# Optimization experiments

Measured on AMD Instinct MI355X. Metric: run time of the kernel, lower is better.

Reference implementation:

```python
import jax, jax.numpy as jnp
import numpy as np

D_MODEL = 1024
N_HEADS = 16
D_HEAD = 64
SEQ = 2048
BATCH = 2
ATTN_SCALE = float(np.sqrt(D_HEAD))  # cfg.use_attn_scale = True
NEG_INF = -1e9


def setup_inputs() -> dict:
    key = jax.random.key(0)
    ks = jax.random.split(key, 8)
    s = 0.02
    return {
        "query_input": jax.random.normal(ks[0], (BATCH, SEQ, D_MODEL), jnp.float32),
        "key_input": jax.random.normal(ks[1], (BATCH, SEQ, D_MODEL), jnp.float32),
        "value_input": jax.random.normal(ks[2], (BATCH, SEQ, D_MODEL), jnp.float32),
        "W_Q": jax.random.normal(ks[3], (N_HEADS, D_MODEL, D_HEAD), jnp.float32) * s,
        "W_K": jax.random.normal(ks[4], (N_HEADS, D_MODEL, D_HEAD), jnp.float32) * s,
        "W_V": jax.random.normal(ks[5], (N_HEADS, D_MODEL, D_HEAD), jnp.float32) * s,
        "W_O": jax.random.normal(ks[6], (N_HEADS, D_HEAD, D_MODEL), jnp.float32) * s,
        "b_Q": jnp.zeros((N_HEADS, D_HEAD), jnp.float32),
        "b_K": jnp.zeros((N_HEADS, D_HEAD), jnp.float32),
        "b_V": jnp.zeros((N_HEADS, D_HEAD), jnp.float32),
        "b_O": jnp.zeros((D_MODEL,), jnp.float32),
    }


def reference(query_input, key_input, value_input, W_Q, W_K, W_V, W_O, b_Q, b_K, b_V, b_O):
    # QKV projections: [batch, pos, d_model] x [head, d_model, d_head] -> [batch, pos, head, d_head]
    q = jnp.einsum("bpd,hde->bphe", query_input, W_Q) + b_Q
    k = jnp.einsum("bpd,hde->bphe", key_input, W_K) + b_K
    v = jnp.einsum("bpd,hde->bphe", value_input, W_V) + b_V

    # attn scores [batch, head, query_pos, key_pos]
    scores = jnp.einsum("bqhe,bkhe->bhqk", q, k) / ATTN_SCALE

    # causal mask (attn_type == 'global'): tril over [n_ctx, n_ctx] sliced to seq
    causal = jnp.tril(jnp.ones((SEQ, SEQ), bool))
    scores = jnp.where(causal[None, None, :, :], scores, NEG_INF)

    pattern = jax.nn.softmax(scores, axis=-1)

    # z: [batch, query_pos, head, d_head]
    z = jnp.einsum("bhqk,bkhe->bqhe", pattern, v)

    # output projection: [batch, pos, d_model]
    out = jnp.einsum("bqhe,hed->bqd", z, W_O) + b_O
    return out
```

## Files before the change

kernel.cpp:

```cpp
#include <hip/hip_runtime.h>
#include <stdint.h>


typedef __attribute__((ext_vector_type(8))) short short8;
typedef __attribute__((ext_vector_type(4))) short short4v;
typedef __attribute__((ext_vector_type(4))) float floatx4;
typedef __attribute__((ext_vector_type(4))) unsigned int uintx4;
typedef __attribute__((ext_vector_type(2))) unsigned int uint2v;

#define MFMA16(a, b, c) __builtin_amdgcn_mfma_f32_16x16x32_bf16(a, b, c, 0, 0, 0)

#if __has_builtin(__builtin_amdgcn_mfma_f32_16x16x16bf16_1k)
#define HAVE_K16 1
#define MFMAK16(a, b, c) __builtin_amdgcn_mfma_f32_16x16x16bf16_1k(a, b, c, 0, 0, 0)
#else
#define HAVE_K16 0
#endif

__device__ __forceinline__ unsigned short f2b(float f) {
  unsigned int u = __builtin_bit_cast(unsigned int, f);
  u = (u + 0x7fffu + ((u >> 16) & 1u)) >> 16;
  return (unsigned short)u;
}
__device__ __forceinline__ float exp2f_fast(float x) {
#if __has_builtin(__builtin_amdgcn_exp2f)
  return __builtin_amdgcn_exp2f(x);
#else
  return exp2f(x);
#endif
}
__device__ __forceinline__ unsigned int pack2_bf16(float lo, float hi) {
#if __has_builtin(__builtin_amdgcn_perm)
  return __builtin_amdgcn_perm(__builtin_bit_cast(unsigned int, hi),
                               __builtin_bit_cast(unsigned int, lo), 0x07060302u);
#else
  return (__builtin_bit_cast(unsigned int, lo) >> 16) |
         (__builtin_bit_cast(unsigned int, hi) & 0xffff0000u);
#endif
}

__device__ __forceinline__ void async_copy16(void* lds, const void* g) {
  __builtin_amdgcn_global_load_lds(
      (const __attribute__((address_space(1))) unsigned int*)g,
      (__attribute__((address_space(3))) unsigned int*)lds, 16, 0, 0);
}

__device__ __forceinline__ void xpose4(floatx4& v, int lane) {
  {
    float s0 = __shfl_xor(v[1], 1, 64);
    float s1 = __shfl_xor(v[0], 1, 64);
    float s2 = __shfl_xor(v[3], 1, 64);
    float s3 = __shfl_xor(v[2], 1, 64);
    if (lane & 1) { v[0] = s0; v[2] = s2; } else { v[1] = s1; v[3] = s3; }
  }
  {
    float s0 = __shfl_xor(v[2], 2, 64);
    float s1 = __shfl_xor(v[3], 2, 64);
    float s2 = __shfl_xor(v[0], 2, 64);
    float s3 = __shfl_xor(v[1], 2, 64);
    if (lane & 2) { v[0] = s0; v[1] = s1; } else { v[2] = s2; v[3] = s3; }
  }
}

__global__ __launch_bounds__(256) void convall(
    const float* __restrict__ Xq, const float* __restrict__ Xk,
    const float* __restrict__ Xv, const float* __restrict__ WQ,
    const float* __restrict__ WK, const float* __restrict__ WV,
    const float* __restrict__ WO, unsigned short* __restrict__ xout,
    unsigned short* __restrict__ wout, unsigned short* __restrict__ woout) {
  __shared__ float T[64][65];
  const int bid = blockIdx.x;
  const int t = threadIdx.x;
  if (bid < 12288) {
    const int yy = bid / 4096, x = bid - yy * 4096;
    const float* in = (yy == 0) ? Xq : ((yy == 1) ? Xk : Xv);
    size_t i = (size_t)x * 256 + t;
    float4 v = ((const float4*)in)[i];
    ushort4 u;
    u.x = f2b(v.x); u.y = f2b(v.y); u.z = f2b(v.z); u.w = f2b(v.w);
    ((ushort4*)(xout + (size_t)yy * 4194304))[i] = u;
    return;
  }
  const int rr = t >> 4, cc = t & 15;
  if (bid < 13056) {
    const int sub = bid - 12288;
    const int yy = sub >> 8, x = sub & 255;
    const float* in = (yy == 0) ? WQ : ((yy == 1) ? WK : WV);
    const int h = x >> 4, d0 = (x & 15) << 6;
#pragma unroll
    for (int it = 0; it < 4; ++it) {
      int dl = it * 16 + rr;
      float4 v = *(const float4*)&in[(size_t)h * 65536 + (size_t)(d0 + dl) * 64 + cc * 4];
      T[dl][cc * 4 + 0] = v.x; T[dl][cc * 4 + 1] = v.y;
      T[dl][cc * 4 + 2] = v.z; T[dl][cc * 4 + 3] = v.w;
    }
    __syncthreads();
    unsigned short* ob = wout + (size_t)yy * 1048576;
#pragma unroll
    for (int it = 0; it < 4; ++it) {
      int e = it * 16 + rr;
      ushort4 u;
      u.x = f2b(T[cc * 4 + 0][e]); u.y = f2b(T[cc * 4 + 1][e]);
      u.z = f2b(T[cc * 4 + 2][e]); u.w = f2b(T[cc * 4 + 3][e]);
      *(ushort4*)&ob[(size_t)(h * 64 + e) * 1024 + d0 + cc * 4] = u;
    }
    return;
  }
  {
    const int x = bid - 13056;
    const int r0 = (x & 15) << 6, c0 = (x >> 4) << 6;
#pragma unroll
    for (int it = 0; it < 4; ++it) {
      int rl = it * 16 + rr;
      float4 v = *(const float4*)&WO[(size_t)(r0 + rl) * 1024 + c0 + cc * 4];
      T[rl][cc * 4 + 0] = v.x; T[rl][cc * 4 + 1] = v.y;
      T[rl][cc * 4 + 2] = v.z; T[rl][cc * 4 + 3] = v.w;
    }
    __syncthreads();
#pragma unroll
    for (int it = 0; it < 4; ++it) {
      int dl = it * 16 + rr;
      ushort4 u;
      u.x = f2b(T[cc * 4 + 0][dl]); u.y = f2b(T[cc * 4 + 1][dl]);
      u.z = f2b(T[cc * 4 + 2][dl]); u.w = f2b(T[cc * 4 + 3][dl]);
      *(ushort4*)&woout[(size_t)(c0 + dl) * 1024 + r0 + cc * 4] = u;
    }
  }
}

template <int TM, int NZ>
__global__ __launch_bounds__(512, (TM == 128) ? 6 : 4) void gemm512(
    const short* __restrict__ A0, const short* __restrict__ A1,
    const short* __restrict__ A2, const short* __restrict__ B0,
    const short* __restrict__ B1, const short* __restrict__ B2,
    const float* __restrict__ bias0, const float* __restrict__ bias1,
    const float* __restrict__ bias2, unsigned short* __restrict__ ob0,
    unsigned short* __restrict__ ob1, unsigned short* __restrict__ ob2,
    float* __restrict__ outf, float qscale) {
  constexpr int WAVES_N = (TM == 128) ? 2 : 4;
  constexpr int NJ = (TM == 128) ? 4 : 2;
  constexpr int NY = 4096 / TM;
  __shared__ short As[TM * 32];
  __shared__ short Bs[128 * 32];

  const int L = blockIdx.x;
  const int x = L / (NY * NZ);
  const int r = L - x * (NY * NZ);
  const int y = r / NZ;
  const int z = r - y * NZ;

  const short* A = (z == 0) ? A0 : (z == 1) ? A1 : A2;
  const short* Bt = (z == 0) ? B0 : (z == 1) ? B1 : B2;

  const int tid = threadIdx.x;
  const int lane = tid & 63, w = tid >> 6;
  const int quad = lane >> 4, col = lane & 15;
  const int m0 = y * TM, n0 = x * 128;
  const int wm = (w / WAVES_N) * 32, wn = (w % WAVES_N) * (NJ * 16);

  floatx4 acc[2][NJ] = {};

  const int lr = lane >> 2, gc = (lane & 3) ^ ((lane >> 3) & 3);
  const short* ga = A + (size_t)(m0 + w * 16 + lr) * 1024 + gc * 8;
  const short* gb = Bt + (size_t)(n0 + w * 16 + lr) * 1024 + gc * 8;
  const int asw = (col >> 1) & 3;
  const bool stageA = (w < TM / 16);

  for (int k0 = 0; k0 < 1024; k0 += 32) {
    if (stageA) async_copy16(&As[(w * 16) * 32], ga);
    async_copy16(&Bs[(w * 16) * 32], gb);
    ga += 32; gb += 32;
    __syncthreads();
    short8 af[2], bf[NJ];
#pragma unroll
    for (int mi = 0; mi < 2; ++mi)
      af[mi] = *(const short8*)&As[(wm + mi * 16 + col) * 32 + ((quad ^ asw) * 8)];
#pragma unroll
    for (int nj = 0; nj < NJ; ++nj)
      bf[nj] = *(const short8*)&Bs[(wn + nj * 16 + col) * 32 + ((quad ^ asw) * 8)];
#pragma unroll
    for (int mi = 0; mi < 2; ++mi)
#pragma unroll
      for (int nj = 0; nj < NJ; ++nj)
        acc[mi][nj] = MFMA16(af[mi], bf[nj], acc[mi][nj]);
    __syncthreads();
  }

  const float* bias = (z == 0) ? bias0 : (z == 1) ? bias1 : bias2;
  unsigned short* outb = (z == 0) ? ob0 : (z == 1) ? ob1 : ob2;
  const int mode = (NZ == 3) ? ((z == 2) ? 2 : 1) : 0;
  const float scale = (NZ == 3 && z == 0) ? qscale : 1.0f;

  float bv[NJ];
#pragma unroll
  for (int nj = 0; nj < NJ; ++nj) bv[nj] = bias[n0 + wn + nj * 16 + col];

  if (mode == 2) {
#pragma unroll
    for (int mi = 0; mi < 2; ++mi)
#pragma unroll
      for (int nj = 0; nj < NJ; ++nj) {
        int m = m0 + wm + mi * 16 + quad * 4;
        int n = n0 + wn + nj * 16 + col;
        int bb = m >> 11, s = m & 2047, h = n >> 6, e = n & 63;
        ushort4 u;
        u.x = f2b(acc[mi][nj][0] + bv[nj]);
        u.y = f2b(acc[mi][nj][1] + bv[nj]);
        u.z = f2b(acc[mi][nj][2] + bv[nj]);
        u.w = f2b(acc[mi][nj][3] + bv[nj]);
        *(ushort4*)&outb[(((size_t)bb * 16 + h) * 64 + e) * 2048 + s] = u;
      }
  } else {
#pragma unroll
    for (int mi = 0; mi < 2; ++mi)
#pragma unroll
      for (int nj = 0; nj < NJ; ++nj) {
        floatx4 v;
#pragma unroll
        for (int rr = 0; rr < 4; ++rr) v[rr] = (acc[mi][nj][rr] + bv[nj]) * scale;
        xpose4(v, lane);
        int m = m0 + wm + mi * 16 + quad * 4 + (col & 3);
        int nb = n0 + wn + nj * 16 + (col & ~3);
        if (mode == 0) {
          *(floatx4*)&outf[(size_t)m * 1024 + nb] = v;
        } else {
          int bb = m >> 11, s = m & 2047, h = nb >> 6, e = nb & 63;
          ushort4 u;
          u.x = f2b(v[0]); u.y = f2b(v[1]); u.z = f2b(v[2]); u.w = f2b(v[3]);
          *(ushort4*)&outb[(((size_t)bb * 16 + h) * 2048 + s) * 64 + e] = u;
        }
      }
  }
}

#if !HAVE_K16
__device__ __forceinline__ void exchange4(const unsigned int* u01,
                                          const unsigned int* u23, int srcA,
                                          int srcB, bool hiq, short8& pf0,
                                          short8& pf1) {
  unsigned int xA0 = (unsigned int)__shfl((int)u01[0], srcA, 64);
  unsigned int xA1 = (unsigned int)__shfl((int)u01[1], srcA, 64);
  unsigned int yA0 = (unsigned int)__shfl((int)u23[0], srcA, 64);
  unsigned int yA1 = (unsigned int)__shfl((int)u23[1], srcA, 64);
  unsigned int xB0 = (unsigned int)__shfl((int)u01[0], srcB, 64);
  unsigned int xB1 = (unsigned int)__shfl((int)u01[1], srcB, 64);
  unsigned int yB0 = (unsigned int)__shfl((int)u23[0], srcB, 64);
  unsigned int yB1 = (unsigned int)__shfl((int)u23[1], srcB, 64);
  uintx4 v0;
  v0.x = hiq ? xA1 : xA0; v0.y = hiq ? yA1 : yA0;
  v0.z = hiq ? xB1 : xB0; v0.w = hiq ? yB1 : yB0;
  pf0 = __builtin_bit_cast(short8, v0);
  xA0 = (unsigned int)__shfl((int)u01[2], srcA, 64);
  xA1 = (unsigned int)__shfl((int)u01[3], srcA, 64);
  yA0 = (unsigned int)__shfl((int)u23[2], srcA, 64);
  yA1 = (unsigned int)__shfl((int)u23[3], srcA, 64);
  xB0 = (unsigned int)__shfl((int)u01[2], srcB, 64);
  xB1 = (unsigned int)__shfl((int)u01[3], srcB, 64);
  yB0 = (unsigned int)__shfl((int)u23[2], srcB, 64);
  yB1 = (unsigned int)__shfl((int)u23[3], srcB, 64);
  uintx4 v1;
  v1.x = hiq ? xA1 : xA0; v1.y = hiq ? yA1 : yA0;
  v1.z = hiq ? xB1 : xB0; v1.w = hiq ? yB1 : yB0;
  pf1 = __builtin_bit_cast(short8, v1);
}
#endif

__device__ __forceinline__ void stage_kv(short* Kbuf, short* Vbuf,
                                         const short* kg, const short* vg,
                                         int kv0, int w, int slr, int sgc) {
  const short* kr = kg + (size_t)(kv0 + w * 16 + slr) * 64 + sgc * 8;
  async_copy16(&Kbuf[(w * 16) * 64], kr);
  async_copy16(&Kbuf[(w * 16 + 8) * 64], kr + 8 * 64);
  const short* vr = vg + (size_t)(w * 16 + slr) * 2048 + kv0 + sgc * 8;
  async_copy16(&Vbuf[(w * 16) * 64], vr);
  async_copy16(&Vbuf[(w * 16 + 8) * 64], vr + 8 * 2048);
}

__global__ __launch_bounds__(256) void attn(const short* __restrict__ q,
                                            const short* __restrict__ k,
                                            const short* __restrict__ vt,
                                            unsigned short* __restrict__ z) {
  __shared__ short Ks[2][64 * 64];
  __shared__ short Vs[2][64 * 64];

  const int tid = threadIdx.x;
  const int lane = tid & 63, w = tid >> 6;
  const int quad = lane >> 4, col = lane & 15;
  const int qt = 31 - (blockIdx.x >> 5), bh = blockIdx.x & 31;
  const int q0 = qt * 64, qw0 = q0 + w * 16;
  const size_t base = (size_t)bh * (2048 * 64);

  const short* qp = q + base + (size_t)(qw0 + col) * 64 + quad * 8;
  short8 bq0 = *(const short8*)qp;
  short8 bq1 = *(const short8*)(qp + 32);

  floatx4 o[4] = {};
  float m_run = -1e30f, l_run = 0.f;

  const short* kg = k + base;
  const short* vg = vt + base;
  const int ksw = col & 7;
  const int slr = lane >> 3, sgc = (lane & 7) ^ slr;
#if !HAVE_K16
  const int srcA = ((quad & 1) << 5) + col, srcB = srcA + 16;
  const bool hiq = (quad & 2) != 0;
#endif

  stage_kv(Ks[0], Vs[0], kg, vg, 0, w, slr, sgc);
  int p = 0;

  for (int t = 0; t <= qt; ++t) {
    __syncthreads();
    if (t < qt) stage_kv(Ks[p ^ 1], Vs[p ^ 1], kg, vg, (t + 1) * 64, w, slr, sgc);

    const bool diag = (t == qt);
    const int mtmax = diag ? w : 3;

    floatx4 st[4];
#pragma unroll
    for (int mt = 0; mt < 4; ++mt) {
      if (mt <= mtmax) {
        const short* kb = &Ks[p][(mt * 16 + col) * 64];
        short8 ka0 = *(const short8*)(kb + (quad ^ ksw) * 8);
        short8 ka1 = *(const short8*)(kb + ((quad + 4) ^ ksw) * 8);
        floatx4 a = {0.f, 0.f, 0.f, 0.f};
        a = MFMA16(ka0, bq0, a);
        a = MFMA16(ka1, bq1, a);
        if (diag && mt == mtmax) {
#pragma unroll
          for (int r = 0; r < 4; ++r)
            if (quad * 4 + r > col) a[r] = -1e9f;
        }
        st[mt] = a;
      }
    }

    float pmax = -3e38f;
#pragma unroll
    for (int mt = 0; mt < 4; ++mt)
      if (mt <= mtmax) {
#pragma unroll
        for (int r = 0; r < 4; ++r) pmax = fmaxf(pmax, st[mt][r]);
      }
    pmax = fmaxf(pmax, __shfl_xor(pmax, 16, 64));
    pmax = fmaxf(pmax, __shfl_xor(pmax, 32, 64));
    float mnew = fmaxf(m_run, pmax);
    float alpha = exp2f_fast(m_run - mnew);
    m_run = mnew;

    unsigned int u01[4], u23[4];
    float lsum = 0.f;
#pragma unroll
    for (int mt = 0; mt < 4; ++mt) {
      if (mt <= mtmax) {
        float p0 = exp2f_fast(st[mt][0] - mnew);
        float p1 = exp2f_fast(st[mt][1] - mnew);
        float p2 = exp2f_fast(st[mt][2] - mnew);
        float p3 = exp2f_fast(st[mt][3] - mnew);
        lsum += (p0 + p1) + (p2 + p3);
        u01[mt] = pack2_bf16(p0, p1);
        u23[mt] = pack2_bf16(p2, p3);
      } else {
        u01[mt] = 0u; u23[mt] = 0u;
      }
    }
    lsum += __shfl_xor(lsum, 16, 64);
    lsum += __shfl_xor(lsum, 32, 64);
    l_run = l_run * alpha + lsum;

#if HAVE_K16
    short4v pb[4];
#pragma unroll
    for (int mt = 0; mt < 4; ++mt) {
      uint2v uu;
      uu.x = u01[mt]; uu.y = u23[mt];
      pb[mt] = __builtin_bit_cast(short4v, uu);
    }
#pragma unroll
    for (int et = 0; et < 4; ++et) {
      const short* vrow = &Vs[p][(et * 16 + col) * 64];
      floatx4 t0 = o[et];
#pragma unroll
      for (int r = 0; r < 4; ++r) t0[r] *= alpha;
#pragma unroll
      for (int mt = 0; mt < 4; ++mt) {
        if (mt <= mtmax) {
          int c = mt * 2 + (quad >> 1);
          short4v va = *(const short4v*)&vrow[((c ^ ksw) * 8) + (quad & 1) * 4];
          t0 = MFMAK16(va, pb[mt], t0);
        }
      }
      o[et] = t0;
    }
#else
    short8 pf0, pf1;
    exchange4(u01, u23, srcA, srcB, hiq, pf0, pf1);
#pragma unroll
    for (int et = 0; et < 4; ++et) {
      const short* vb = &Vs[p][(et * 16 + col) * 64];
      short8 va0 = *(const short8*)(vb + (quad ^ ksw) * 8);
      short8 va1 = *(const short8*)(vb + ((quad + 4) ^ ksw) * 8);
      floatx4 t0 = o[et];
#pragma unroll
      for (int r = 0; r < 4; ++r) t0[r] *= alpha;
      t0 = MFMA16(va0, pf0, t0);
      t0 = MFMA16(va1, pf1, t0);
      o[et] = t0;
    }
#endif
    p ^= 1;
  }

  const int b = bh >> 4, h = bh & 15;
#if __has_builtin(__builtin_amdgcn_rcpf)
  const float invl = __builtin_amdgcn_rcpf(l_run);
#else
  const float invl = 1.f / l_run;
#endif
  unsigned short* zr = z + (((size_t)b * 2048 + qw0 + col) * 16 + h) * 64;
#pragma unroll
  for (int et = 0; et < 4; ++et) {
    ushort4 u;
    u.x = f2b(o[et][0] * invl); u.y = f2b(o[et][1] * invl);
    u.z = f2b(o[et][2] * invl); u.w = f2b(o[et][3] * invl);
    *(ushort4*)&zr[et * 16 + quad * 4] = u;
  }
}

extern "C" void kernel_launch(void* const* d_in, const int* in_sizes, int n_in,
                              void* d_out, int out_size, void* d_ws, size_t ws_size,
                              hipStream_t stream) {
  (void)in_sizes; (void)n_in; (void)out_size; (void)ws_size;
  const float* Xq = (const float*)d_in[0];
  const float* Xk = (const float*)d_in[1];
  const float* Xv = (const float*)d_in[2];
  const float* WQ = (const float*)d_in[3];
  const float* WK = (const float*)d_in[4];
  const float* WV = (const float*)d_in[5];
  const float* WO = (const float*)d_in[6];
  const float* bQ = (const float*)d_in[7];
  const float* bK = (const float*)d_in[8];
  const float* bV = (const float*)d_in[9];
  const float* bO = (const float*)d_in[10];
  float* out = (float*)d_out;

  unsigned short* xqb = (unsigned short*)d_ws;
  unsigned short* xkb = xqb + 4194304;
  unsigned short* xvb = xkb + 4194304;
  unsigned short* wqt = xvb + 4194304;
  unsigned short* wkt = wqt + 1048576;
  unsigned short* wvt = wkt + 1048576;
  unsigned short* wot = wvt + 1048576;
  unsigned short* qb = wot + 1048576;
  unsigned short* kb = qb + 4194304;
  unsigned short* vtb = kb + 4194304;
  unsigned short* zb = vtb + 4194304;

  convall<<<13312, 256, 0, stream>>>(Xq, Xk, Xv, WQ, WK, WV, WO, xqb, wqt, wot);

  const float qscale = 0.125f * 1.44269504088896f;
  gemm512<128, 3><<<768, 512, 0, stream>>>(
      (const short*)xqb, (const short*)xkb, (const short*)xvb,
      (const short*)wqt, (const short*)wkt, (const short*)wvt, bQ, bK, bV, qb,
      kb, vtb, nullptr, qscale);

  attn<<<1024, 256, 0, stream>>>((const short*)qb, (const short*)kb,
                                 (const short*)vtb, zb);

  gemm512<64, 1><<<512, 512, 0, stream>>>(
      (const short*)zb, (const short*)zb, (const short*)zb, (const short*)wot,
      (const short*)wot, (const short*)wot, bO, bO, bO, nullptr, nullptr,
      nullptr, out, 1.0f);
}
```

Before: 221.3 us.

## Fuse fp32-to-bf16 activation conversion into QKV GEMM and pair causal query tiles

Drops the separate activation conversion pass: the QKV GEMM now loads fp32 inputs directly, converts them to bf16 in registers with a register-prefetch of the next k-slice, and writes them to LDS. This removes a full write and re-read of bf16 copies of the three inputs. The attention kernel now runs 512-thread blocks that each pair a long and a short causal query tile (qt and 31-qt), sharing K/V staging, which balances work across blocks and halves the grid. The trade-offs are synchronous fp32 loads instead of async LDS copies in the GEMM, and idle waves in the short-tile half once it passes its diagonal.

```diff
diff --git a/kernel.cpp b/kernel.cpp
--- a/kernel.cpp
+++ b/kernel.cpp
@@ -36,6 +36,15 @@
 #else
   return (__builtin_bit_cast(unsigned int, lo) >> 16) |
          (__builtin_bit_cast(unsigned int, hi) & 0xffff0000u);
+#endif
+}
+__device__ __forceinline__ unsigned int pack2_bf16_rnd(float lo, float hi) {
+  unsigned int ul = __builtin_bit_cast(unsigned int, lo) + 0x8000u;
+  unsigned int uh = __builtin_bit_cast(unsigned int, hi) + 0x8000u;
+#if __has_builtin(__builtin_amdgcn_perm)
+  return __builtin_amdgcn_perm(uh, ul, 0x07060302u);
+#else
+  return (ul >> 16) | (uh & 0xffff0000u);
 #endif
 }
 
@@ -62,29 +71,15 @@
   }
 }
 
-__global__ __launch_bounds__(256) void convall(
-    const float* __restrict__ Xq, const float* __restrict__ Xk,
-    const float* __restrict__ Xv, const float* __restrict__ WQ,
-    const float* __restrict__ WK, const float* __restrict__ WV,
-    const float* __restrict__ WO, unsigned short* __restrict__ xout,
+__global__ __launch_bounds__(256) void convw(
+    const float* __restrict__ WQ, const float* __restrict__ WK,
+    const float* __restrict__ WV, const float* __restrict__ WO,
     unsigned short* __restrict__ wout, unsigned short* __restrict__ woout) {
   __shared__ float T[64][65];
   const int bid = blockIdx.x;
-  const int t = threadIdx.x;
-  if (bid < 12288) {
-    const int yy = bid / 4096, x = bid - yy * 4096;
-    const float* in = (yy == 0) ? Xq : ((yy == 1) ? Xk : Xv);
-    size_t i = (size_t)x * 256 + t;
-    float4 v = ((const float4*)in)[i];
-    ushort4 u;
-    u.x = f2b(v.x); u.y = f2b(v.y); u.z = f2b(v.z); u.w = f2b(v.w);
-    ((ushort4*)(xout + (size_t)yy * 4194304))[i] = u;
-    return;
-  }
-  const int rr = t >> 4, cc = t & 15;
-  if (bid < 13056) {
-    const int sub = bid - 12288;
-    const int yy = sub >> 8, x = sub & 255;
+  const int t = threadIdx.x, rr = t >> 4, cc = t & 15;
+  if (bid < 768) {
+    const int yy = bid >> 8, x = bid & 255;
     const float* in = (yy == 0) ? WQ : ((yy == 1) ? WK : WV);
     const int h = x >> 4, d0 = (x & 15) << 6;
 #pragma unroll
@@ -107,7 +102,7 @@
     return;
   }
   {
-    const int x = bid - 13056;
+    const int x = bid - 768;
     const int r0 = (x & 15) << 6, c0 = (x >> 4) << 6;
 #pragma unroll
     for (int it = 0; it < 4; ++it) {
@@ -128,10 +123,10 @@
   }
 }
 
-template <int TM, int NZ>
+template <int TM, int NZ, bool AFP32>
 __global__ __launch_bounds__(512, (TM == 128) ? 6 : 4) void gemm512(
-    const short* __restrict__ A0, const short* __restrict__ A1,
-    const short* __restrict__ A2, const short* __restrict__ B0,
+    const void* __restrict__ A0, const void* __restrict__ A1,
+    const void* __restrict__ A2, const short* __restrict__ B0,
     const short* __restrict__ B1, const short* __restrict__ B2,
     const float* __restrict__ bias0, const float* __restrict__ bias1,
     const float* __restrict__ bias2, unsigned short* __restrict__ ob0,
@@ -149,7 +144,7 @@
   const int y = r / NZ;
   const int z = r - y * NZ;
 
-  const short* A = (z == 0) ? A0 : (z == 1) ? A1 : A2;
+  const void* Av = (z == 0) ? A0 : (z == 1) ? A1 : A2;
   const short* Bt = (z == 0) ? B0 : (z == 1) ? B1 : B2;
 
   const int tid = threadIdx.x;
@@ -161,15 +156,41 @@
   floatx4 acc[2][NJ] = {};
 
   const int lr = lane >> 2, gc = (lane & 3) ^ ((lane >> 3) & 3);
-  const short* ga = A + (size_t)(m0 + w * 16 + lr) * 1024 + gc * 8;
   const short* gb = Bt + (size_t)(n0 + w * 16 + lr) * 1024 + gc * 8;
   const int asw = (col >> 1) & 3;
-  const bool stageA = (w < TM / 16);
+
+  const short* ga = nullptr;
+  const float* gaf = nullptr;
+  float4 pa0, pa1;
+  if (AFP32) {
+    gaf = (const float*)Av + (size_t)(m0 + w * 16 + lr) * 1024 + gc * 8;
+    pa0 = *(const float4*)gaf;
+    pa1 = *(const float4*)(gaf + 4);
+    gaf += 32;
+  } else {
+    ga = (const short*)Av + (size_t)(m0 + w * 16 + lr) * 1024 + gc * 8;
+  }
+  const bool stageA = AFP32 || (w < TM / 16);
 
   for (int k0 = 0; k0 < 1024; k0 += 32) {
-    if (stageA) async_copy16(&As[(w * 16) * 32], ga);
+    if (AFP32) {
+      uintx4 pk;
+      pk.x = pack2_bf16_rnd(pa0.x, pa0.y);
+      pk.y = pack2_bf16_rnd(pa0.z, pa0.w);
+      pk.z = pack2_bf16_rnd(pa1.x, pa1.y);
+      pk.w = pack2_bf16_rnd(pa1.z, pa1.w);
+      *(uintx4*)&As[(w * 16 + lr) * 32 + (lane & 3) * 8] = pk;
+      if (k0 + 32 < 1024) {
+        pa0 = *(const float4*)gaf;
+        pa1 = *(const float4*)(gaf + 4);
+        gaf += 32;
+      }
+    } else if (stageA) {
+      async_copy16(&As[(w * 16) * 32], ga);
+      ga += 32;
+    }
     async_copy16(&Bs[(w * 16) * 32], gb);
-    ga += 32; gb += 32;
+    gb += 32;
     __syncthreads();
     short8 af[2], bf[NJ];
 #pragma unroll
@@ -265,18 +286,16 @@
 }
 #endif
 
-__device__ __forceinline__ void stage_kv(short* Kbuf, short* Vbuf,
-                                         const short* kg, const short* vg,
-                                         int kv0, int w, int slr, int sgc) {
-  const short* kr = kg + (size_t)(kv0 + w * 16 + slr) * 64 + sgc * 8;
-  async_copy16(&Kbuf[(w * 16) * 64], kr);
-  async_copy16(&Kbuf[(w * 16 + 8) * 64], kr + 8 * 64);
-  const short* vr = vg + (size_t)(w * 16 + slr) * 2048 + kv0 + sgc * 8;
-  async_copy16(&Vbuf[(w * 16) * 64], vr);
-  async_copy16(&Vbuf[(w * 16 + 8) * 64], vr + 8 * 2048);
-}
-
-__global__ __launch_bounds__(256) void attn(const short* __restrict__ q,
+__device__ __forceinline__ void stage_kv8(short* Kbuf, short* Vbuf,
+                                          const short* kg, const short* vg,
+                                          int kv0, int w, int slr, int sgc) {
+  const short* kr = kg + (size_t)(kv0 + w * 8 + slr) * 64 + sgc * 8;
+  async_copy16(&Kbuf[(w * 8) * 64], kr);
+  const short* vr = vg + (size_t)(w * 8 + slr) * 2048 + kv0 + sgc * 8;
+  async_copy16(&Vbuf[(w * 8) * 64], vr);
+}
+
+__global__ __launch_bounds__(512) void attn(const short* __restrict__ q,
                                             const short* __restrict__ k,
                                             const short* __restrict__ vt,
                                             unsigned short* __restrict__ z) {
@@ -286,8 +305,12 @@
   const int tid = threadIdx.x;
   const int lane = tid & 63, w = tid >> 6;
   const int quad = lane >> 4, col = lane & 15;
-  const int qt = 31 - (blockIdx.x >> 5), bh = blockIdx.x & 31;
-  const int q0 = qt * 64, qw0 = q0 + w * 16;
+  const int ip = blockIdx.x >> 5, bh = blockIdx.x & 31;
+  const int qtA = 31 - ip;
+  const int qtB = ip;
+  const int wt = w >> 2, wq = w & 3;
+  const int myqt = wt ? qtB : qtA;
+  const int qw0 = myqt * 64 + wq * 16;
   const size_t base = (size_t)bh * (2048 * 64);
 
   const short* qp = q + base + (size_t)(qw0 + col) * 64 + quad * 8;
@@ -306,108 +329,110 @@
   const bool hiq = (quad & 2) != 0;
 #endif
 
-  stage_kv(Ks[0], Vs[0], kg, vg, 0, w, slr, sgc);
+  stage_kv8(Ks[0], Vs[0], kg, vg, 0, w, slr, sgc);
   int p = 0;
 
-  for (int t = 0; t <= qt; ++t) {
+  for (int t = 0; t <= qtA; ++t) {
     __syncthreads();
-    if (t < qt) stage_kv(Ks[p ^ 1], Vs[p ^ 1], kg, vg, (t + 1) * 64, w, slr, sgc);
-
-    const bool diag = (t == qt);
-    const int mtmax = diag ? w : 3;
-
-    floatx4 st[4];
-#pragma unroll
-    for (int mt = 0; mt < 4; ++mt) {
-      if (mt <= mtmax) {
-        const short* kb = &Ks[p][(mt * 16 + col) * 64];
-        short8 ka0 = *(const short8*)(kb + (quad ^ ksw) * 8);
-        short8 ka1 = *(const short8*)(kb + ((quad + 4) ^ ksw) * 8);
-        floatx4 a = {0.f, 0.f, 0.f, 0.f};
-        a = MFMA16(ka0, bq0, a);
-        a = MFMA16(ka1, bq1, a);
-        if (diag && mt == mtmax) {
-#pragma unroll
-          for (int r = 0; r < 4; ++r)
-            if (quad * 4 + r > col) a[r] = -1e9f;
-        }
-        st[mt] = a;
-      }
-    }
-
-    float pmax = -3e38f;
-#pragma unroll
-    for (int mt = 0; mt < 4; ++mt)
-      if (mt <= mtmax) {
-#pragma unroll
-        for (int r = 0; r < 4; ++r) pmax = fmaxf(pmax, st[mt][r]);
-      }
-    pmax = fmaxf(pmax, __shfl_xor(pmax, 16, 64));
-    pmax = fmaxf(pmax, __shfl_xor(pmax, 32, 64));
-    float mnew = fmaxf(m_run, pmax);
-    float alpha = exp2f_fast(m_run - mnew);
-    m_run = mnew;
-
-    unsigned int u01[4], u23[4];
-    float lsum = 0.f;
-#pragma unroll
-    for (int mt = 0; mt < 4; ++mt) {
-      if (mt <= mtmax) {
-        float p0 = exp2f_fast(st[mt][0] - mnew);
-        float p1 = exp2f_fast(st[mt][1] - mnew);
-        float p2 = exp2f_fast(st[mt][2] - mnew);
-        float p3 = exp2f_fast(st[mt][3] - mnew);
-        lsum += (p0 + p1) + (p2 + p3);
-        u01[mt] = pack2_bf16(p0, p1);
-        u23[mt] = pack2_bf16(p2, p3);
-      } else {
-        u01[mt] = 0u; u23[mt] = 0u;
-      }
-    }
-    lsum += __shfl_xor(lsum, 16, 64);
-    lsum += __shfl_xor(lsum, 32, 64);
-    l_run = l_run * alpha + lsum;
-
-#if HAVE_K16
-    short4v pb[4];
-#pragma unroll
-    for (int mt = 0; mt < 4; ++mt) {
-      uint2v uu;
-      uu.x = u01[mt]; uu.y = u23[mt];
-      pb[mt] = __builtin_bit_cast(short4v, uu);
-    }
-#pragma unroll
-    for (int et = 0; et < 4; ++et) {
-      const short* vrow = &Vs[p][(et * 16 + col) * 64];
-      floatx4 t0 = o[et];
-#pragma unroll
-      for (int r = 0; r < 4; ++r) t0[r] *= alpha;
+    if (t < qtA) stage_kv8(Ks[p ^ 1], Vs[p ^ 1], kg, vg, (t + 1) * 64, w, slr, sgc);
+
+    if (t <= myqt) {
+      const bool diag = (t == myqt);
+      const int mtmax = diag ? wq : 3;
+
+      floatx4 st[4];
 #pragma unroll
       for (int mt = 0; mt < 4; ++mt) {
         if (mt <= mtmax) {
-          int c = mt * 2 + (quad >> 1);
-          short4v va = *(const short4v*)&vrow[((c ^ ksw) * 8) + (quad & 1) * 4];
-          t0 = MFMAK16(va, pb[mt], t0);
+          const short* kb = &Ks[p][(mt * 16 + col) * 64];
+          short8 ka0 = *(const short8*)(kb + (quad ^ ksw) * 8);
+          short8 ka1 = *(const short8*)(kb + ((quad + 4) ^ ksw) * 8);
+          floatx4 a = {0.f, 0.f, 0.f, 0.f};
+          a = MFMA16(ka0, bq0, a);
+          a = MFMA16(ka1, bq1, a);
+          if (diag && mt == mtmax) {
+#pragma unroll
+            for (int r = 0; r < 4; ++r)
+              if (quad * 4 + r > col) a[r] = -1e9f;
+          }
+          st[mt] = a;
         }
       }
-      o[et] = t0;
-    }
-#else
-    short8 pf0, pf1;
-    exchange4(u01, u23, srcA, srcB, hiq, pf0, pf1);
-#pragma unroll
-    for (int et = 0; et < 4; ++et) {
-      const short* vb = &Vs[p][(et * 16 + col) * 64];
-      short8 va0 = *(const short8*)(vb + (quad ^ ksw) * 8);
-      short8 va1 = *(const short8*)(vb + ((quad + 4) ^ ksw) * 8);
-      floatx4 t0 = o[et];
-#pragma unroll
-      for (int r = 0; r < 4; ++r) t0[r] *= alpha;
-      t0 = MFMA16(va0, pf0, t0);
-      t0 = MFMA16(va1, pf1, t0);
-      o[et] = t0;
-    }
-#endif
+
+      float pmax = -3e38f;
+#pragma unroll
+      for (int mt = 0; mt < 4; ++mt)
+        if (mt <= mtmax) {
+#pragma unroll
+          for (int r = 0; r < 4; ++r) pmax = fmaxf(pmax, st[mt][r]);
+        }
+      pmax = fmaxf(pmax, __shfl_xor(pmax, 16, 64));
+      pmax = fmaxf(pmax, __shfl_xor(pmax, 32, 64));
+      float mnew = fmaxf(m_run, pmax);
+      float alpha = exp2f_fast(m_run - mnew);
+      m_run = mnew;
+
+      unsigned int u01[4], u23[4];
+      float lsum = 0.f;
+#pragma unroll
+      for (int mt = 0; mt < 4; ++mt) {
+        if (mt <= mtmax) {
+          float p0 = exp2f_fast(st[mt][0] - mnew);
+          float p1 = exp2f_fast(st[mt][1] - mnew);
+          float p2 = exp2f_fast(st[mt][2] - mnew);
+          float p3 = exp2f_fast(st[mt][3] - mnew);
+          lsum += (p0 + p1) + (p2 + p3);
+          u01[mt] = pack2_bf16(p0, p1);
+          u23[mt] = pack2_bf16(p2, p3);
+        } else {
+          u01[mt] = 0u; u23[mt] = 0u;
+        }
+      }
+      lsum += __shfl_xor(lsum, 16, 64);
+      lsum += __shfl_xor(lsum, 32, 64);
+      l_run = l_run * alpha + lsum;
+
+#if HAVE_K16
+      short4v pb[4];
+#pragma unroll
+      for (int mt = 0; mt < 4; ++mt) {
+        uint2v uu;
+        uu.x = u01[mt]; uu.y = u23[mt];
+        pb[mt] = __builtin_bit_cast(short4v, uu);
+      }
+#pragma unroll
+      for (int et = 0; et < 4; ++et) {
+        const short* vrow = &Vs[p][(et * 16 + col) * 64];
+        floatx4 t0 = o[et];
+#pragma unroll
+        for (int r = 0; r < 4; ++r) t0[r] *= alpha;
+#pragma unroll
+        for (int mt = 0; mt < 4; ++mt) {
+          if (mt <= mtmax) {
+            int c = mt * 2 + (quad >> 1);
+            short4v va = *(const short4v*)&vrow[((c ^ ksw) * 8) + (quad & 1) * 4];
+            t0 = MFMAK16(va, pb[mt], t0);
+          }
+        }
+        o[et] = t0;
+      }
+#else
+      short8 pf0, pf1;
+      exchange4(u01, u23, srcA, srcB, hiq, pf0, pf1);
+#pragma unroll
+      for (int et = 0; et < 4; ++et) {
+        const short* vb = &Vs[p][(et * 16 + col) * 64];
+        short8 va0 = *(const short8*)(vb + (quad ^ ksw) * 8);
+        short8 va1 = *(const short8*)(vb + ((quad + 4) ^ ksw) * 8);
+        floatx4 t0 = o[et];
+#pragma unroll
+        for (int r = 0; r < 4; ++r) t0[r] *= alpha;
+        t0 = MFMA16(va0, pf0, t0);
+        t0 = MFMA16(va1, pf1, t0);
+        o[et] = t0;
+      }
+#endif
+    }
     p ^= 1;
   }
 
@@ -444,10 +469,7 @@
   const float* bO = (const float*)d_in[10];
   float* out = (float*)d_out;
 
-  unsigned short* xqb = (unsigned short*)d_ws;
-  unsigned short* xkb = xqb + 4194304;
-  unsigned short* xvb = xkb + 4194304;
-  unsigned short* wqt = xvb + 4194304;
+  unsigned short* wqt = (unsigned short*)d_ws;
   unsigned short* wkt = wqt + 1048576;
   unsigned short* wvt = wkt + 1048576;
   unsigned short* wot = wvt + 1048576;
@@ -456,19 +478,17 @@
   unsigned short* vtb = kb + 4194304;
   unsigned short* zb = vtb + 4194304;
 
-  convall<<<13312, 256, 0, stream>>>(Xq, Xk, Xv, WQ, WK, WV, WO, xqb, wqt, wot);
+  convw<<<1024, 256, 0, stream>>>(WQ, WK, WV, WO, wqt, wot);
 
   const float qscale = 0.125f * 1.44269504088896f;
-  gemm512<128, 3><<<768, 512, 0, stream>>>(
-      (const short*)xqb, (const short*)xkb, (const short*)xvb,
-      (const short*)wqt, (const short*)wkt, (const short*)wvt, bQ, bK, bV, qb,
-      kb, vtb, nullptr, qscale);
-
-  attn<<<1024, 256, 0, stream>>>((const short*)qb, (const short*)kb,
-                                 (const short*)vtb, zb);
-
-  gemm512<64, 1><<<512, 512, 0, stream>>>(
-      (const short*)zb, (const short*)zb, (const short*)zb, (const short*)wot,
-      (const short*)wot, (const short*)wot, bO, bO, bO, nullptr, nullptr,
-      nullptr, out, 1.0f);
-}
+  gemm512<128, 3, true><<<768, 512, 0, stream>>>(
+      Xq, Xk, Xv, (const short*)wqt, (const short*)wkt, (const short*)wvt, bQ,
+      bK, bV, qb, kb, vtb, nullptr, qscale);
+
+  attn<<<512, 512, 0, stream>>>((const short*)qb, (const short*)kb,
+                                (const short*)vtb, zb);
+
+  gemm512<64, 1, false><<<512, 512, 0, stream>>>(
+      zb, zb, zb, (const short*)wot, (const short*)wot, (const short*)wot, bO,
+      bO, bO, nullptr, nullptr, nullptr, out, 1.0f);
+}
```

Result: slower. 266.3 us (+20.3%).
